# Kernel optimization log

Hardware: AMD Instinct MI355X
Metric: run time of the kernel (lower is better)

The kernel has to match this reference:

```python
import jax, jax.numpy as jnp
import numpy as np
from jax import lax

NUM_HEADS = 8
HEAD_DIM = 32
DIM = NUM_HEADS * HEAD_DIM  # 256
SR = 2
B, H, W = 4, 64, 64


def setup_inputs() -> dict:
    key = jax.random.key(0)
    ks = jax.random.split(key, 6)
    x = jax.random.normal(ks[0], (B, DIM, H, W), dtype=jnp.float32)
    # query: 1x1 conv without bias -> plain [out,in] matrix
    Wq = jax.random.normal(ks[1], (DIM, DIM), dtype=jnp.float32) * (1.0 / np.sqrt(DIM))
    # key/value: sr x sr conv, stride sr, no bias (OIHW)
    Wk = jax.random.normal(ks[2], (DIM, DIM, SR, SR), dtype=jnp.float32) * (1.0 / np.sqrt(DIM * SR * SR))
    Wv = jax.random.normal(ks[3], (DIM, DIM, SR, SR), dtype=jnp.float32) * (1.0 / np.sqrt(DIM * SR * SR))
    rel_h = jax.random.normal(ks[4], (1, NUM_HEADS, HEAD_DIM, 1, H // SR), dtype=jnp.float32)
    rel_w = jax.random.normal(ks[5], (1, NUM_HEADS, HEAD_DIM, W // SR, 1), dtype=jnp.float32)
    return {"x": x, "Wq": Wq, "Wk": Wk, "Wv": Wv, "rel_h": rel_h, "rel_w": rel_w}


def reference(x, Wq, Wk, Wv, rel_h, rel_w):
    b, c, h, w = x.shape
    nh, hd = NUM_HEADS, HEAD_DIM
    scale = hd ** (-0.5)
    dn = ('NCHW', 'OIHW', 'NCHW')

    # q: 1x1 conv == channel matmul; [B, C, H*W] -> [B, nh, hd, Nq]
    q = jnp.einsum('oc,bchw->bohw', Wq, x).reshape(b, nh, hd, h * w)
    # k, v: sr x sr conv, stride sr -> [B, nh, hd, Nkv]
    k = lax.conv_general_dilated(x, Wk, window_strides=(SR, SR), padding='VALID',
                                 dimension_numbers=dn).reshape(b, nh, hd, -1)
    v = lax.conv_general_dilated(x, Wv, window_strides=(SR, SR), padding='VALID',
                                 dimension_numbers=dn).reshape(b, nh, hd, -1)

    # attn scores: q^T k -> [B, nh, Nq, Nkv]
    attn = jnp.einsum('bhdn,bhdm->bhnm', q, k)
    # relative positional bias: (rel_h + rel_w) broadcast -> [nh, hd, Nkv]
    pos = (rel_h + rel_w).reshape(nh, hd, -1)
    attn = attn + jnp.einsum('bhdn,hdm->bhnm', q, pos)
    attn = jax.nn.softmax(attn * scale, axis=-1)

    # out = v @ attn^T -> [B, nh, hd, Nq] -> [B, C, H, W]
    out = jnp.einsum('bhdm,bhnm->bhdn', v, attn).reshape(b, c, h, w)
    return out
```

## Files before the change

kernel.cpp:

```cpp
#include <hip/hip_runtime.h>
#include <math.h>


typedef __bf16 bf16;
typedef __attribute__((ext_vector_type(4))) __bf16 bf16x4;
typedef __attribute__((ext_vector_type(8))) __bf16 bf16x8;
typedef __attribute__((ext_vector_type(4))) float f32x4;
typedef __attribute__((ext_vector_type(2))) __fp16 fp16x2_raw;
typedef __attribute__((ext_vector_type(4))) _Float16 f16x4;
typedef __attribute__((ext_vector_type(8))) _Float16 f16x8;

#define MFMA16 __builtin_amdgcn_mfma_f32_16x16x32_bf16
#define MFMA16H32 __builtin_amdgcn_mfma_f32_16x16x32_f16

#define QSCALE 0.25503486f
#define SOFTMAX_SHIFT 10.0f
#define VSTR 136

__global__ void k_prep_w(const float* __restrict__ Wq, const float* __restrict__ Wk,
                         const float* __restrict__ Wv,
                         bf16* __restrict__ Wq_bf, bf16* __restrict__ Wkv_bf) {
    int tid = blockIdx.x * 256 + threadIdx.x;
    if (tid < 32768) {
        int c = tid >> 6, i4 = (tid & 63) * 4;
        const float* Wsrc = (c < 256) ? Wk : Wv;
        int cs = c & 255;
        f32x4 r[4];
#pragma unroll
        for (int j = 0; j < 4; j++)
            r[j] = ((const f32x4*)Wsrc)[cs * 256 + i4 + j];
#pragma unroll
        for (int tap = 0; tap < 4; tap++) {
            bf16x4 o;
#pragma unroll
            for (int j = 0; j < 4; j++) o[j] = (bf16)r[j][tap];
            *(bf16x4*)(Wkv_bf + c * 1024 + tap * 256 + i4) = o;
        }
    } else {
        int q = tid - 32768;
        f32x4 q4 = ((const f32x4*)Wq)[q];
        bf16x4 o;
#pragma unroll
        for (int e = 0; e < 4; e++) o[e] = (bf16)(q4[e] * QSCALE);
        *(bf16x4*)(Wq_bf + q * 4) = o;
    }
}

__global__ void k_xT(const float* __restrict__ x, bf16* __restrict__ xT) {
    int b = blockIdx.z, c0 = blockIdx.y * 64, n0 = blockIdx.x * 64;
    __shared__ float tile[64][65];
    int t = threadIdx.x;
    const float* xp = x + (size_t)(b * 256 + c0) * 4096 + n0;
#pragma unroll
    for (int it = 0; it < 4; it++) {
        int u = it * 256 + t;
        int row = u >> 4, colq = u & 15;
        f32x4 v = *(const f32x4*)(xp + (size_t)row * 4096 + colq * 4);
#pragma unroll
        for (int e = 0; e < 4; e++) tile[row][colq * 4 + e] = v[e];
    }
    __syncthreads();
    bf16* op = xT + (size_t)(b * 4096 + n0) * 256 + c0;
#pragma unroll
    for (int it = 0; it < 2; it++) {
        int u = it * 256 + t;
        int orow = u >> 3, oc8 = (u & 7) * 8;
        bf16x8 o;
#pragma unroll
        for (int e = 0; e < 8; e++) o[e] = (bf16)tile[oc8 + e][orow];
        *(bf16x8*)(op + (size_t)orow * 256 + oc8) = o;
    }
}

__launch_bounds__(256)
__global__ void k_gemm_kv(const bf16* __restrict__ xT, const bf16* __restrict__ Wkv_bf,
                          const float* __restrict__ rel_h, const float* __restrict__ rel_w,
                          bf16* __restrict__ kpos_t, _Float16* __restrict__ v_td) {
    int b = blockIdx.z;
    int bx = blockIdx.x;
    int m0 = bx * 32;
    int c0w = blockIdx.y * 64 + (threadIdx.x >> 6) * 16;
    int t = threadIdx.x, l = t & 63;
    int lr = l & 15, lg = l >> 4;
    __shared__ __align__(16) bf16 Ps[2][32 * 264];
    const bf16* xb = xT + (size_t)b * 4096 * 256;
    int srow = t >> 3;
    int scu0 = (t & 7) * 4;
    uint4 pre[4];
#define LOAD_CHUNK(tap)                                                        \
    {                                                                          \
        int dy = (tap) >> 1, dx = (tap) & 1;                                   \
        const bf16* src = xb + (size_t)((2 * bx + dy) * 64 + 2 * srow + dx) * 256; \
        _Pragma("unroll")                                                      \
        for (int j = 0; j < 4; j++)                                            \
            pre[j] = *(const uint4*)(src + (scu0 + j) * 8);                    \
    }
#define WRITE_CHUNK(buf)                                                       \
    {                                                                          \
        bf16* dst = Ps[buf] + srow * 264 + scu0 * 8;                           \
        _Pragma("unroll")                                                      \
        for (int j = 0; j < 4; j++) *(uint4*)(dst + j * 8) = pre[j];           \
    }
    LOAD_CHUNK(0)
    WRITE_CHUNK(0)
    const bf16* Gkb = Wkv_bf + (size_t)(c0w + lr) * 1024 + lg * 8;
    const bf16* Gvb = Gkb + 256 * 1024;
    f32x4 accK[2] = {}, accV[2] = {};
    for (int ch = 0; ch < 4; ch++) {
        if (ch < 3) LOAD_CHUNK(ch + 1)
        __syncthreads();
        const bf16* P = Ps[ch & 1];
#pragma unroll
        for (int kk = 0; kk < 8; kk++) {
            bf16x8 pa0 = *(const bf16x8*)(P + lr * 264 + kk * 32 + lg * 8);
            bf16x8 pa1 = *(const bf16x8*)(P + (16 + lr) * 264 + kk * 32 + lg * 8);
            bf16x8 gk = *(const bf16x8*)(Gkb + ch * 256 + kk * 32);
            bf16x8 gv = *(const bf16x8*)(Gvb + ch * 256 + kk * 32);
            accK[0] = MFMA16(pa0, gk, accK[0], 0, 0, 0);
            accK[1] = MFMA16(pa1, gk, accK[1], 0, 0, 0);
            accV[0] = MFMA16(gv, pa0, accV[0], 0, 0, 0);
            accV[1] = MFMA16(gv, pa1, accV[1], 0, 0, 0);
        }
        if (ch < 3) {
            __syncthreads();
            WRITE_CHUNK((ch + 1) & 1)
        }
    }
    {
        int cc = c0w + lr;
        float rw = rel_w[cc * 32 + bx];
#pragma unroll
        for (int i = 0; i < 2; i++)
#pragma unroll
            for (int r = 0; r < 4; r++) {
                int ml = i * 16 + lg * 4 + r;
                float val = accK[i][r] + rw + rel_h[cc * 32 + ml];
                kpos_t[((size_t)(b * 8 + (cc >> 5)) * 1024 + m0 + ml) * 32 + (cc & 31)] = (bf16)val;
            }
    }
#pragma unroll
    for (int j = 0; j < 2; j++) {
        int m = m0 + j * 16 + lr;
#pragma unroll
        for (int r = 0; r < 4; r++) {
            int cc = c0w + lg * 4 + r;
            v_td[((size_t)(b * 8 + (cc >> 5)) * 32 + (cc & 31)) * 1024 + m] = (_Float16)accV[j][r];
        }
    }
#undef LOAD_CHUNK
#undef WRITE_CHUNK
}

__launch_bounds__(256, 4)
__global__ void k_attn(const bf16* __restrict__ xT, const bf16* __restrict__ Wq_bf,
                       const bf16* __restrict__ kpos_t, const _Float16* __restrict__ v_td,
                       float* __restrict__ out) {
    int b = blockIdx.z, h = blockIdx.y;
    int t = threadIdx.x;
    int w = t >> 6, l = t & 63;
    int n0 = blockIdx.x * 128 + w * 32;
    int lr = l & 15, lg = l >> 4;
    const size_t bh = (size_t)(b * 8 + h);
    __shared__ __align__(16) char smem[16384 + 2 * 32 * VSTR * 2];
    bf16* KsB = (bf16*)smem;
    _Float16* VsB = (_Float16*)(smem + 16384);
    const bf16* Kb = kpos_t + bh * 1024 * 32;
    const _Float16* Vb = v_td + bh * 32 * 1024;
    uint4 pk_r0, pk_r1, pv_r0, pv_r1;
#define LOADCH(ch)                                                             \
    {                                                                          \
        const uint4* ksrc = (const uint4*)(Kb + (size_t)(ch) * 128 * 32);      \
        pk_r0 = ksrc[t];                                                       \
        pk_r1 = ksrc[t + 256];                                                 \
        pv_r0 = *(const uint4*)(Vb + (size_t)(t >> 4) * 1024 + (ch) * 128 +    \
                                (t & 15) * 8);                                 \
        pv_r1 = *(const uint4*)(Vb + (size_t)((t + 256) >> 4) * 1024 +         \
                                (ch) * 128 + (t & 15) * 8);                    \
    }
#define KWR(uu, reg)                                                           \
    {                                                                          \
        int m = (uu) >> 2;                                                     \
        int mb = m & 31;                                                       \
        int jl = ((mb >> 3) << 2) + (mb & 3) + ((mb >> 2) & 1) * 16;           \
        int prow = (m & ~31) + jl;                                             \
        int phys = ((prow >> 1) + ((uu) & 3)) & 3;                             \
        *(uint4*)(&KsB[(buf_) * 4096 + prow * 32 + phys * 8]) = reg;           \
    }
#define WRITECH(buf)                                                           \
    {                                                                          \
        const int buf_ = (buf);                                                \
        KWR(t, pk_r0)                                                          \
        KWR(t + 256, pk_r1)                                                    \
        *(uint4*)(&VsB[buf_ * (32 * VSTR) + (t >> 4) * VSTR + (t & 15) * 8]) = pv_r0; \
        *(uint4*)(&VsB[buf_ * (32 * VSTR) + ((t + 256) >> 4) * VSTR + (t & 15) * 8]) = pv_r1; \
    }
    LOADCH(0)
    bf16* Qs = (bf16*)smem + w * 1280;
    bf16x8 bq0, bq1;
    {
        const bf16* Aw = Wq_bf + (size_t)(h * 32 + lr) * 256 + lg * 8;
        const bf16* Bx = xT + (size_t)(b * 4096 + n0 + lr) * 256 + lg * 8;
        f32x4 aq[2][2] = {};
#pragma unroll
        for (int kk = 0; kk < 8; kk++) {
            bf16x8 a0 = *(const bf16x8*)(Aw + kk * 32);
            bf16x8 a1 = *(const bf16x8*)(Aw + 16 * 256 + kk * 32);
            bf16x8 b0 = *(const bf16x8*)(Bx + kk * 32);
            bf16x8 b1 = *(const bf16x8*)(Bx + 16 * 256 + kk * 32);
            aq[0][0] = MFMA16(a0, b0, aq[0][0], 0, 0, 0);
            aq[0][1] = MFMA16(a0, b1, aq[0][1], 0, 0, 0);
            aq[1][0] = MFMA16(a1, b0, aq[1][0], 0, 0, 0);
            aq[1][1] = MFMA16(a1, b1, aq[1][1], 0, 0, 0);
        }
#pragma unroll
        for (int i = 0; i < 2; i++)
#pragma unroll
            for (int j = 0; j < 2; j++) {
                bf16x4 pk;
#pragma unroll
                for (int r = 0; r < 4; r++) pk[r] = (bf16)aq[i][j][r];
                *(bf16x4*)(Qs + (j * 16 + lr) * 40 + i * 16 + lg * 4) = pk;
            }
        bf16x4 a0 = *(const bf16x4*)(Qs + lr * 40 + lg * 8);
        bf16x4 a1 = *(const bf16x4*)(Qs + lr * 40 + lg * 8 + 4);
        bf16x4 b0 = *(const bf16x4*)(Qs + (16 + lr) * 40 + lg * 8);
        bf16x4 b1 = *(const bf16x4*)(Qs + (16 + lr) * 40 + lg * 8 + 4);
#pragma unroll
        for (int e = 0; e < 4; e++) {
            bq0[e] = a0[e]; bq0[4 + e] = a1[e];
            bq1[e] = b0[e]; bq1[4 + e] = b1[e];
        }
    }
    __syncthreads();
    WRITECH(0)
    LOADCH(1)
    __syncthreads();
    f32x4 accO[2][2] = {};
    f32x4 accS[2] = {};
    const f16x8 ones8 = {(_Float16)1.f, (_Float16)1.f, (_Float16)1.f, (_Float16)1.f,
                         (_Float16)1.f, (_Float16)1.f, (_Float16)1.f, (_Float16)1.f};
    const f32x4 zs = {-SOFTMAX_SHIFT, -SOFTMAX_SHIFT, -SOFTMAX_SHIFT, -SOFTMAX_SHIFT};
    const int koff = (((lr >> 1) + lg) & 3) * 8;
    for (int ch = 0; ch < 8; ch++) {
        const bf16* Kc = KsB + (ch & 1) * 4096;
        const _Float16* Vc = VsB + (ch & 1) * (32 * VSTR);
        __builtin_amdgcn_s_setprio(1);
#pragma unroll
        for (int kb = 0; kb < 4; kb++) {
            bf16x8 ak0 = *(const bf16x8*)(Kc + (kb * 32 + lr) * 32 + koff);
            bf16x8 ak1 = *(const bf16x8*)(Kc + (kb * 32 + 16 + lr) * 32 + koff);
            f16x8 v0 = *(const f16x8*)(Vc + lr * VSTR + kb * 32 + lg * 8);
            f16x8 v1 = *(const f16x8*)(Vc + (16 + lr) * VSTR + kb * 32 + lg * 8);
            {
                f32x4 s0 = MFMA16(ak0, bq0, zs, 0, 0, 0);
                f32x4 s1 = MFMA16(ak1, bq0, zs, 0, 0, 0);
                f16x8 pa;
                fp16x2_raw c01 = __builtin_amdgcn_cvt_pkrtz(
                    __builtin_amdgcn_exp2f(s0[0]), __builtin_amdgcn_exp2f(s0[1]));
                fp16x2_raw c23 = __builtin_amdgcn_cvt_pkrtz(
                    __builtin_amdgcn_exp2f(s0[2]), __builtin_amdgcn_exp2f(s0[3]));
                fp16x2_raw c45 = __builtin_amdgcn_cvt_pkrtz(
                    __builtin_amdgcn_exp2f(s1[0]), __builtin_amdgcn_exp2f(s1[1]));
                fp16x2_raw c67 = __builtin_amdgcn_cvt_pkrtz(
                    __builtin_amdgcn_exp2f(s1[2]), __builtin_amdgcn_exp2f(s1[3]));
                pa[0] = c01[0]; pa[1] = c01[1]; pa[2] = c23[0]; pa[3] = c23[1];
                pa[4] = c45[0]; pa[5] = c45[1]; pa[6] = c67[0]; pa[7] = c67[1];
                accO[0][0] = MFMA16H32(pa, v0, accO[0][0], 0, 0, 0);
                accO[0][1] = MFMA16H32(pa, v1, accO[0][1], 0, 0, 0);
                accS[0]    = MFMA16H32(pa, ones8, accS[0], 0, 0, 0);
            }
            {
                f32x4 s0 = MFMA16(ak0, bq1, zs, 0, 0, 0);
                f32x4 s1 = MFMA16(ak1, bq1, zs, 0, 0, 0);
                f16x8 pa;
                fp16x2_raw c01 = __builtin_amdgcn_cvt_pkrtz(
                    __builtin_amdgcn_exp2f(s0[0]), __builtin_amdgcn_exp2f(s0[1]));
                fp16x2_raw c23 = __builtin_amdgcn_cvt_pkrtz(
                    __builtin_amdgcn_exp2f(s0[2]), __builtin_amdgcn_exp2f(s0[3]));
                fp16x2_raw c45 = __builtin_amdgcn_cvt_pkrtz(
                    __builtin_amdgcn_exp2f(s1[0]), __builtin_amdgcn_exp2f(s1[1]));
                fp16x2_raw c67 = __builtin_amdgcn_cvt_pkrtz(
                    __builtin_amdgcn_exp2f(s1[2]), __builtin_amdgcn_exp2f(s1[3]));
                pa[0] = c01[0]; pa[1] = c01[1]; pa[2] = c23[0]; pa[3] = c23[1];
                pa[4] = c45[0]; pa[5] = c45[1]; pa[6] = c67[0]; pa[7] = c67[1];
                accO[1][0] = MFMA16H32(pa, v0, accO[1][0], 0, 0, 0);
                accO[1][1] = MFMA16H32(pa, v1, accO[1][1], 0, 0, 0);
                accS[1]    = MFMA16H32(pa, ones8, accS[1], 0, 0, 0);
            }
        }
        __builtin_amdgcn_s_setprio(0);
        if (ch < 7) {
            WRITECH((ch + 1) & 1)
            if (ch < 6) LOADCH(ch + 2)
            __syncthreads();
        }
    }
#undef LOADCH
#undef KWR
#undef WRITECH
#pragma unroll
    for (int hq = 0; hq < 2; hq++) {
        float inv[4];
#pragma unroll
        for (int r = 0; r < 4; r++) inv[r] = 1.0f / accS[hq][r];
#pragma unroll
        for (int dt = 0; dt < 2; dt++) {
            int c = h * 32 + dt * 16 + lr;
            float* op = out + (size_t)(b * 256 + c) * 4096 + n0 + hq * 16 + lg * 4;
            f32x4 o;
#pragma unroll
            for (int r = 0; r < 4; r++) o[r] = accO[hq][dt][r] * inv[r];
            *(f32x4*)op = o;
        }
    }
}

extern "C" void kernel_launch(void* const* d_in, const int* in_sizes, int n_in,
                              void* d_out, int out_size, void* d_ws, size_t ws_size,
                              hipStream_t stream) {
    const float* x    = (const float*)d_in[0];
    const float* Wq   = (const float*)d_in[1];
    const float* Wk   = (const float*)d_in[2];
    const float* Wv   = (const float*)d_in[3];
    const float* relh = (const float*)d_in[4];
    const float* relw = (const float*)d_in[5];
    float* out = (float*)d_out;
    char* ws = (char*)d_ws;

    bf16*      xT     = (bf16*)(ws);
    bf16*      kposT  = (bf16*)(ws + (8u << 20));
    _Float16*  v_td   = (_Float16*)(ws + (10u << 20));
    bf16*      Wq_bf  = (bf16*)(ws + (12u << 20));
    bf16*      Wkv_bf = (bf16*)(ws + (12u << 20) + (256u << 10));

    k_prep_w <<<192,            256, 0, stream>>>(Wq, Wk, Wv, Wq_bf, Wkv_bf);
    k_xT     <<<dim3(64, 4, 4), 256, 0, stream>>>(x, xT);
    k_gemm_kv<<<dim3(32, 4, 4), 256, 0, stream>>>(xT, Wkv_bf, relh, relw, kposT, v_td);
    k_attn   <<<dim3(32, 8, 4), 256, 0, stream>>>(xT, Wq_bf, kposT, v_td, out);
}
```

Baseline: 141.4 us.

## Double per-warp query tile in attention kernel to reuse K/V loads

Each warp in k_attn now handles 64 queries instead of 32, using four query sub-tiles that share the same K and V fragments loaded from LDS. The grid shrinks from 32 to 16 blocks in x, so each staged K/V chunk is loaded once per 256 queries. The aim is to cut global and LDS traffic and synchronisation per unit of work. In exchange, register pressure roughly doubles for the accumulators, launch bounds drop to 2 blocks per SM, and only 512 blocks remain, which lowers occupancy and latency hiding. Qs now spans 4 warps × 2560 bf16 (20 KB), which overflows the 16 KB K region and runs into the V region. This is safe only because a __syncthreads separates the Q-staging reads from WRITECH(0).

```diff
diff --git a/kernel.cpp b/kernel.cpp
--- a/kernel.cpp
+++ b/kernel.cpp
@@ -151,14 +151,14 @@
 #undef WRITE_CHUNK
 }
 
-__launch_bounds__(256, 4)
+__launch_bounds__(256, 2)
 __global__ void k_attn(const bf16* __restrict__ xT, const bf16* __restrict__ Wq_bf,
                        const bf16* __restrict__ kpos_t, const _Float16* __restrict__ v_td,
                        float* __restrict__ out) {
     int b = blockIdx.z, h = blockIdx.y;
     int t = threadIdx.x;
     int w = t >> 6, l = t & 63;
-    int n0 = blockIdx.x * 128 + w * 32;
+    int n0 = blockIdx.x * 256 + w * 64;
     int lr = l & 15, lg = l >> 4;
     const size_t bh = (size_t)(b * 8 + h);
     __shared__ __align__(16) char smem[16384 + 2 * 32 * VSTR * 2];
@@ -195,48 +195,46 @@
         *(uint4*)(&VsB[buf_ * (32 * VSTR) + ((t + 256) >> 4) * VSTR + (t & 15) * 8]) = pv_r1; \
     }
     LOADCH(0)
-    bf16* Qs = (bf16*)smem + w * 1280;
-    bf16x8 bq0, bq1;
+    bf16* Qs = (bf16*)smem + w * 2560;
+    bf16x8 bq[4];
     {
         const bf16* Aw = Wq_bf + (size_t)(h * 32 + lr) * 256 + lg * 8;
         const bf16* Bx = xT + (size_t)(b * 4096 + n0 + lr) * 256 + lg * 8;
-        f32x4 aq[2][2] = {};
+        f32x4 aq[2][4] = {};
 #pragma unroll
         for (int kk = 0; kk < 8; kk++) {
             bf16x8 a0 = *(const bf16x8*)(Aw + kk * 32);
             bf16x8 a1 = *(const bf16x8*)(Aw + 16 * 256 + kk * 32);
-            bf16x8 b0 = *(const bf16x8*)(Bx + kk * 32);
-            bf16x8 b1 = *(const bf16x8*)(Bx + 16 * 256 + kk * 32);
-            aq[0][0] = MFMA16(a0, b0, aq[0][0], 0, 0, 0);
-            aq[0][1] = MFMA16(a0, b1, aq[0][1], 0, 0, 0);
-            aq[1][0] = MFMA16(a1, b0, aq[1][0], 0, 0, 0);
-            aq[1][1] = MFMA16(a1, b1, aq[1][1], 0, 0, 0);
+#pragma unroll
+            for (int jq = 0; jq < 4; jq++) {
+                bf16x8 bv = *(const bf16x8*)(Bx + (size_t)jq * 16 * 256 + kk * 32);
+                aq[0][jq] = MFMA16(a0, bv, aq[0][jq], 0, 0, 0);
+                aq[1][jq] = MFMA16(a1, bv, aq[1][jq], 0, 0, 0);
+            }
         }
 #pragma unroll
         for (int i = 0; i < 2; i++)
 #pragma unroll
-            for (int j = 0; j < 2; j++) {
+            for (int jq = 0; jq < 4; jq++) {
                 bf16x4 pk;
 #pragma unroll
-                for (int r = 0; r < 4; r++) pk[r] = (bf16)aq[i][j][r];
-                *(bf16x4*)(Qs + (j * 16 + lr) * 40 + i * 16 + lg * 4) = pk;
+                for (int r = 0; r < 4; r++) pk[r] = (bf16)aq[i][jq][r];
+                *(bf16x4*)(Qs + (jq * 16 + lr) * 40 + i * 16 + lg * 4) = pk;
             }
-        bf16x4 a0 = *(const bf16x4*)(Qs + lr * 40 + lg * 8);
-        bf16x4 a1 = *(const bf16x4*)(Qs + lr * 40 + lg * 8 + 4);
-        bf16x4 b0 = *(const bf16x4*)(Qs + (16 + lr) * 40 + lg * 8);
-        bf16x4 b1 = *(const bf16x4*)(Qs + (16 + lr) * 40 + lg * 8 + 4);
-#pragma unroll
-        for (int e = 0; e < 4; e++) {
-            bq0[e] = a0[e]; bq0[4 + e] = a1[e];
-            bq1[e] = b0[e]; bq1[4 + e] = b1[e];
+#pragma unroll
+        for (int jq = 0; jq < 4; jq++) {
+            bf16x4 a0 = *(const bf16x4*)(Qs + (jq * 16 + lr) * 40 + lg * 8);
+            bf16x4 a1 = *(const bf16x4*)(Qs + (jq * 16 + lr) * 40 + lg * 8 + 4);
+#pragma unroll
+            for (int e = 0; e < 4; e++) { bq[jq][e] = a0[e]; bq[jq][4 + e] = a1[e]; }
         }
     }
     __syncthreads();
     WRITECH(0)
     LOADCH(1)
     __syncthreads();
-    f32x4 accO[2][2] = {};
-    f32x4 accS[2] = {};
+    f32x4 accO[4][2] = {};
+    f32x4 accS[4] = {};
     const f16x8 ones8 = {(_Float16)1.f, (_Float16)1.f, (_Float16)1.f, (_Float16)1.f,
                          (_Float16)1.f, (_Float16)1.f, (_Float16)1.f, (_Float16)1.f};
     const f32x4 zs = {-SOFTMAX_SHIFT, -SOFTMAX_SHIFT, -SOFTMAX_SHIFT, -SOFTMAX_SHIFT};
@@ -251,9 +249,10 @@
             bf16x8 ak1 = *(const bf16x8*)(Kc + (kb * 32 + 16 + lr) * 32 + koff);
             f16x8 v0 = *(const f16x8*)(Vc + lr * VSTR + kb * 32 + lg * 8);
             f16x8 v1 = *(const f16x8*)(Vc + (16 + lr) * VSTR + kb * 32 + lg * 8);
-            {
-                f32x4 s0 = MFMA16(ak0, bq0, zs, 0, 0, 0);
-                f32x4 s1 = MFMA16(ak1, bq0, zs, 0, 0, 0);
+#pragma unroll
+            for (int jq = 0; jq < 4; jq++) {
+                f32x4 s0 = MFMA16(ak0, bq[jq], zs, 0, 0, 0);
+                f32x4 s1 = MFMA16(ak1, bq[jq], zs, 0, 0, 0);
                 f16x8 pa;
                 fp16x2_raw c01 = __builtin_amdgcn_cvt_pkrtz(
                     __builtin_amdgcn_exp2f(s0[0]), __builtin_amdgcn_exp2f(s0[1]));
@@ -265,27 +264,9 @@
                     __builtin_amdgcn_exp2f(s1[2]), __builtin_amdgcn_exp2f(s1[3]));
                 pa[0] = c01[0]; pa[1] = c01[1]; pa[2] = c23[0]; pa[3] = c23[1];
                 pa[4] = c45[0]; pa[5] = c45[1]; pa[6] = c67[0]; pa[7] = c67[1];
-                accO[0][0] = MFMA16H32(pa, v0, accO[0][0], 0, 0, 0);
-                accO[0][1] = MFMA16H32(pa, v1, accO[0][1], 0, 0, 0);
-                accS[0]    = MFMA16H32(pa, ones8, accS[0], 0, 0, 0);
-            }
-            {
-                f32x4 s0 = MFMA16(ak0, bq1, zs, 0, 0, 0);
-                f32x4 s1 = MFMA16(ak1, bq1, zs, 0, 0, 0);
-                f16x8 pa;
-                fp16x2_raw c01 = __builtin_amdgcn_cvt_pkrtz(
-                    __builtin_amdgcn_exp2f(s0[0]), __builtin_amdgcn_exp2f(s0[1]));
-                fp16x2_raw c23 = __builtin_amdgcn_cvt_pkrtz(
-                    __builtin_amdgcn_exp2f(s0[2]), __builtin_amdgcn_exp2f(s0[3]));
-                fp16x2_raw c45 = __builtin_amdgcn_cvt_pkrtz(
-                    __builtin_amdgcn_exp2f(s1[0]), __builtin_amdgcn_exp2f(s1[1]));
-                fp16x2_raw c67 = __builtin_amdgcn_cvt_pkrtz(
-                    __builtin_amdgcn_exp2f(s1[2]), __builtin_amdgcn_exp2f(s1[3]));
-                pa[0] = c01[0]; pa[1] = c01[1]; pa[2] = c23[0]; pa[3] = c23[1];
-                pa[4] = c45[0]; pa[5] = c45[1]; pa[6] = c67[0]; pa[7] = c67[1];
-                accO[1][0] = MFMA16H32(pa, v0, accO[1][0], 0, 0, 0);
-                accO[1][1] = MFMA16H32(pa, v1, accO[1][1], 0, 0, 0);
-                accS[1]    = MFMA16H32(pa, ones8, accS[1], 0, 0, 0);
+                accO[jq][0] = MFMA16H32(pa, v0, accO[jq][0], 0, 0, 0);
+                accO[jq][1] = MFMA16H32(pa, v1, accO[jq][1], 0, 0, 0);
+                accS[jq]    = MFMA16H32(pa, ones8, accS[jq], 0, 0, 0);
             }
         }
         __builtin_amdgcn_s_setprio(0);
@@ -299,17 +280,17 @@
 #undef KWR
 #undef WRITECH
 #pragma unroll
-    for (int hq = 0; hq < 2; hq++) {
+    for (int jq = 0; jq < 4; jq++) {
         float inv[4];
 #pragma unroll
-        for (int r = 0; r < 4; r++) inv[r] = 1.0f / accS[hq][r];
+        for (int r = 0; r < 4; r++) inv[r] = 1.0f / accS[jq][r];
 #pragma unroll
         for (int dt = 0; dt < 2; dt++) {
             int c = h * 32 + dt * 16 + lr;
-            float* op = out + (size_t)(b * 256 + c) * 4096 + n0 + hq * 16 + lg * 4;
+            float* op = out + (size_t)(b * 256 + c) * 4096 + n0 + jq * 16 + lg * 4;
             f32x4 o;
 #pragma unroll
-            for (int r = 0; r < 4; r++) o[r] = accO[hq][dt][r] * inv[r];
+            for (int r = 0; r < 4; r++) o[r] = accO[jq][dt][r] * inv[r];
             *(f32x4*)op = o;
         }
     }
@@ -336,5 +317,5 @@
     k_prep_w <<<192,            256, 0, stream>>>(Wq, Wk, Wv, Wq_bf, Wkv_bf);
     k_xT     <<<dim3(64, 4, 4), 256, 0, stream>>>(x, xT);
     k_gemm_kv<<<dim3(32, 4, 4), 256, 0, stream>>>(xT, Wkv_bf, relh, relw, kposT, v_td);
-    k_attn   <<<dim3(32, 8, 4), 256, 0, stream>>>(xT, Wq_bf, kposT, v_td, out);
-}
+    k_attn   <<<dim3(16, 8, 4), 256, 0, stream>>>(xT, Wq_bf, kposT, v_td, out);
+}
```

Result: no change. 142.6 us (+0.9%).
